# Kernel tuning notes

Measured on AMD Instinct MI355X. Metric: run time of the kernel, lower is better.

## Reference

```python
import jax, jax.numpy as jnp
import numpy as np

B, T, D, H = 2, 2048, 1024, 16
HD = D // H
FF = 4 * D
EPS = 1e-5


def rmsnorm(x, w):
    var = jnp.mean(jnp.square(x), axis=-1, keepdims=True)
    return x * jax.lax.rsqrt(var + EPS) * w


def setup_inputs() -> dict:
    key = jax.random.key(0)
    ks = jax.random.split(key, 17)
    sc = 0.02
    d = {}
    d["x"] = jax.random.normal(ks[0], (B, T, D), jnp.float32)
    d["x_token"] = jax.random.normal(ks[1], (B, T, D), jnp.float32)
    d["pos_emb"] = jax.random.normal(ks[2], (T, D), jnp.float32)
    d["lc_weight"] = jax.random.normal(ks[3], (1,), jnp.float32)
    d["Wq"] = jax.random.normal(ks[4], (D, D), jnp.float32) * sc  # per-head query weights stacked
    d["Wk"] = jax.random.normal(ks[5], (D, D), jnp.float32) * sc
    d["Wv"] = jax.random.normal(ks[6], (D, D), jnp.float32) * sc
    d["proj_w"] = jax.random.normal(ks[7], (D, D), jnp.float32) * sc
    d["proj_b"] = jnp.zeros((D,), jnp.float32)
    d["w1_w"] = jax.random.normal(ks[8], (FF, D), jnp.float32) * sc
    d["w1_b"] = jnp.zeros((FF,), jnp.float32)
    d["w2_w"] = jax.random.normal(ks[9], (D, FF), jnp.float32) * sc
    d["w2_b"] = jnp.zeros((D,), jnp.float32)
    d["w3_w"] = jax.random.normal(ks[10], (FF, D), jnp.float32) * sc
    d["w3_b"] = jnp.zeros((FF,), jnp.float32)
    d["norm1_w"] = jnp.ones((D,), jnp.float32)
    d["norm2_w"] = jnp.ones((D,), jnp.float32)
    return d


def reference(x, x_token, pos_emb, lc_weight, Wq, Wk, Wv, proj_w, proj_b,
              w1_w, w1_b, w2_w, w2_b, w3_w, w3_b, norm1_w, norm2_w):
    lc = jax.nn.sigmoid(lc_weight)  # scalar gate
    x_att = lc * x + (1.0 - lc) * x_token
    xn = rmsnorm(x_att, norm1_w)

    # q, v from normed gated input; k from raw positional embedding (faithful to source)
    q = (xn @ Wq.T).reshape(B, T, H, HD)
    k = (pos_emb @ Wk.T).reshape(T, H, HD)
    v = (xn @ Wv.T).reshape(B, T, H, HD)

    # NOTE: scale uses full model dim E (=D), not head_size, as in the source
    scores = jnp.einsum('bqhd,khd->bhqk', q, k) * (D ** -0.5)
    causal = jnp.tril(jnp.ones((T, T), bool))
    scores = jnp.where(causal, scores, -jnp.inf)
    p = jax.nn.softmax(scores, axis=-1)
    attn = jnp.einsum('bhqk,bkhd->bqhd', p, v).reshape(B, T, D)

    x = x + attn @ proj_w.T + proj_b

    xn2 = rmsnorm(x, norm2_w)
    h = jax.nn.silu(xn2 @ w1_w.T + w1_b) * (xn2 @ w3_w.T + w3_b)
    return x + h @ w2_w.T + w2_b
```

## Files before the change

kernel.cpp:

```cpp
#include <hip/hip_runtime.h>
#include <hip/hip_bf16.h>


typedef __hip_bfloat16 bf16;
typedef __attribute__((ext_vector_type(8))) short bf16x8;
typedef __attribute__((ext_vector_type(4))) float floatx4;

constexpr int cB = 2, cT = 2048, cD = 1024, cH = 16, cFF = 4096;
constexpr float cEPS = 1e-5f;
constexpr unsigned BF16_ONES = 0x3F803F80u;

__device__ __forceinline__ float b2f(bf16 x) { return __bfloat162float(x); }
__device__ __forceinline__ bf16  f2b(float x) { return __float2bfloat16(x); }
__device__ __forceinline__ unsigned short f2bu(float x) {
  bf16 t = __float2bfloat16(x);
  union { bf16 b; unsigned short u; } cv;
  cv.b = t;
  return cv.u;
}
__device__ __forceinline__ float loadR(const bf16* p)  { return b2f(*p); }
__device__ __forceinline__ float loadR(const float* p) { return *p; }

__device__ __forceinline__ void gload16(const bf16* g, unsigned short* l) {
  __builtin_amdgcn_global_load_lds(
      (const __attribute__((address_space(1))) void*)g,
      (__attribute__((address_space(3))) void*)l, 16, 0, 0);
}

__device__ __forceinline__ int xcd_remap1(int lin, int n) {
  return (lin & 7) * (n >> 3) + (lin >> 3);
}

struct ConvArgs {
  const void* src[17];
  bf16* dst[17];
  int n[17];
  int sb[17];
};

__global__ __launch_bounds__(256) void convert_all_k(ConvArgs a) {
  const int bid = blockIdx.x;
  int seg = 0;
#pragma unroll
  for (int i = 1; i < 17; i++) seg = (bid >= a.sb[i]) ? i : seg;
  const int n = a.n[seg];
  const int i0 = (bid - a.sb[seg]) * 2048 + threadIdx.x * 8;
  if (i0 >= n) return;
  const bool isb = (((const unsigned*)a.src[15])[0] == BF16_ONES);
  const void* src = a.src[seg];
  bf16* dst = a.dst[seg];
  if (i0 + 8 <= n) {
    if (isb) {
      *(int4*)(dst + i0) = *(const int4*)((const bf16*)src + i0);
    } else {
      float4 f0 = *(const float4*)((const float*)src + i0);
      float4 f1 = *(const float4*)((const float*)src + i0 + 4);
      int4 ro;
      bf16* po = (bf16*)&ro;
      po[0] = f2b(f0.x); po[1] = f2b(f0.y); po[2] = f2b(f0.z); po[3] = f2b(f0.w);
      po[4] = f2b(f1.x); po[5] = f2b(f1.y); po[6] = f2b(f1.z); po[7] = f2b(f1.w);
      *(int4*)(dst + i0) = ro;
    }
  } else {
    for (int j = i0; j < n; j++)
      dst[j] = isb ? ((const bf16*)src)[j] : f2b(((const float*)src)[j]);
  }
}

template <int OUTK, typename ResT>
__device__ __forceinline__ void gemm_core64(
    const bf16* __restrict__ A, const bf16* __restrict__ W,
    const bf16* __restrict__ bias, const ResT* __restrict__ R,
    void* __restrict__ Cv,
    int N, int Kst, int kb, int klen, int m0, int n0,
    unsigned short* As, unsigned short* Bs)
{
  const int tid  = threadIdx.x;
  const int wave = tid >> 6;
  const int lane = tid & 63;
  const int l15  = lane & 15;
  const int quad = lane >> 4;
  const int wm   = (wave >> 1) * 64;
  const int wn   = (wave & 1) * 32;

  const int lr  = lane >> 2;
  const int lc8 = (lane & 3) * 8;
  const bf16* Ag0 = A + (size_t)(m0 + wave * 32 + lr) * Kst + kb + lc8;
  const bf16* Ag1 = Ag0 + (size_t)16 * Kst;
  const bf16* Bg0 = W + (size_t)(n0 + wave * 16 + lr) * Kst + kb + lc8;
  unsigned short* lA0 = &As[(wave * 32) * 32];
  unsigned short* lA1 = &As[(wave * 32 + 16) * 32];
  unsigned short* lB0 = &Bs[(wave * 16) * 32];

  floatx4 acc[4][2];
#pragma unroll
  for (int i = 0; i < 4; i++)
#pragma unroll
    for (int j = 0; j < 2; j++) acc[i][j] = (floatx4){0.f, 0.f, 0.f, 0.f};

  for (int k0 = 0; k0 < klen; k0 += 64) {
    gload16(Ag0 + k0, lA0);
    gload16(Ag1 + k0, lA1);
    gload16(Ag0 + k0 + 32, lA0 + 128 * 32);
    gload16(Ag1 + k0 + 32, lA1 + 128 * 32);
    gload16(Bg0 + k0, lB0);
    gload16(Bg0 + k0 + 32, lB0 + 64 * 32);
    __syncthreads();

    bf16x8 a[4][2], b[2][2];
#pragma unroll
    for (int t = 0; t < 4; t++)
#pragma unroll
      for (int kh = 0; kh < 2; kh++)
        a[t][kh] = *(const bf16x8*)&As[kh * 128 * 32 + (wm + t * 16 + l15) * 32 + quad * 8];
#pragma unroll
    for (int u = 0; u < 2; u++)
#pragma unroll
      for (int kh = 0; kh < 2; kh++)
        b[u][kh] = *(const bf16x8*)&Bs[kh * 64 * 32 + (wn + u * 16 + l15) * 32 + quad * 8];
#pragma unroll
    for (int tm = 0; tm < 4; tm++)
#pragma unroll
      for (int tn = 0; tn < 2; tn++)
#pragma unroll
        for (int kh = 0; kh < 2; kh++)
          acc[tm][tn] = __builtin_amdgcn_mfma_f32_16x16x32_bf16(a[tm][kh], b[tn][kh], acc[tm][tn], 0, 0, 0);
    __syncthreads();
  }

#pragma unroll
  for (int tm = 0; tm < 4; tm++) {
#pragma unroll
    for (int tn = 0; tn < 2; tn++) {
      const int row = m0 + wm + tm * 16 + quad * 4;
      const int col = n0 + wn + tn * 16 + l15;
      float bv = (OUTK != 3 && bias) ? b2f(bias[col]) : 0.f;
#pragma unroll
      for (int i = 0; i < 4; i++) {
        float val = acc[tm][tn][i] + bv;
        const size_t cidx = (size_t)(row + i) * N + col;
        if (OUTK == 3) {
          atomicAdd((float*)Cv + cidx, val);
        } else if (OUTK == 4) {
          ((bf16*)Cv)[(size_t)col * (size_t)(cB * cT) + (row + i)] = f2b(val);
        } else {
          if (R) val += loadR(&R[cidx]);
          if (OUTK == 0) ((bf16*)Cv)[cidx] = f2b(val);
          else           ((float*)Cv)[cidx] = val;
        }
      }
    }
  }
}

template <int OUTK, typename ResT>
__global__ __launch_bounds__(256) void gemm_f(
    const bf16* __restrict__ A, const bf16* __restrict__ W,
    const bf16* __restrict__ bias, const ResT* __restrict__ R,
    void* __restrict__ Cv, int N, int Kst, int kchunk, int gx, int gxy)
{
  __shared__ __align__(16) unsigned short As[2 * 128 * 32];
  __shared__ __align__(16) unsigned short Bs[2 * 64 * 32];
  const int lin = xcd_remap1(blockIdx.x, gridDim.x);
  const int kz  = lin / gxy;
  const int rem = lin % gxy;
  gemm_core64<OUTK, ResT>(A, W, bias, R, Cv, N, Kst, kz * kchunk, kchunk,
                          (rem / gx) * 128, (rem % gx) * 64, As, Bs);
}

__global__ __launch_bounds__(256) void gemm_qkv(
    const bf16* __restrict__ xn, const bf16* __restrict__ pos,
    const bf16* __restrict__ Wq, const bf16* __restrict__ Wv,
    const bf16* __restrict__ Wk,
    bf16* __restrict__ q, bf16* __restrict__ vT, bf16* __restrict__ kb)
{
  __shared__ __align__(16) unsigned short As[2 * 128 * 32];
  __shared__ __align__(16) unsigned short Bs[2 * 64 * 32];
  const int lin = xcd_remap1(blockIdx.x, gridDim.x);
  int z, local;
  if (lin < 512)       { z = 0; local = lin; }
  else if (lin < 1024) { z = 1; local = lin - 512; }
  else                 { z = 2; local = lin - 1024; }
  const int gx = 16;
  const int by = local / gx, bx = local % gx;
  if (z == 1) {
    gemm_core64<4, bf16>(xn, Wv, nullptr, (const bf16*)nullptr, vT,
                         cD, cD, 0, cD, by * 128, bx * 64, As, Bs);
  } else {
    const bf16* A = (z == 2) ? pos : xn;
    const bf16* W = (z == 0) ? Wq : Wk;
    bf16* C = (z == 0) ? q : kb;
    gemm_core64<0, bf16>(A, W, nullptr, (const bf16*)nullptr, C,
                         cD, cD, 0, cD, by * 128, bx * 64, As, Bs);
  }
}

template <int MODE>
__global__ __launch_bounds__(512, 2) void gemm8p(
    const bf16* __restrict__ A, const bf16* __restrict__ W,
    const bf16* __restrict__ bias, bf16* H)
{
  __shared__ __align__(16) unsigned short As[2 * 2 * 256 * 32];
  __shared__ __align__(16) unsigned short Bs[2 * 2 * 256 * 32];
  constexpr int K = cD;
  constexpr int NT = K / 64;
  const int lin = xcd_remap1(blockIdx.x, gridDim.x);
  const int by = lin >> 4, bx = lin & 15;
  const int m0 = by * 256, n0 = bx * 256;

  const int tid  = threadIdx.x;
  const int wave = tid >> 6;
  const int lane = tid & 63;
  const int l15  = lane & 15;
  const int quad = lane >> 4;
  const int wm   = wave >> 2;
  const int wq   = wave & 3;
  const int swz  = (quad ^ (l15 & 3) ^ ((l15 >> 2) & 3)) * 8;

  const int srow = wave * 32 + (lane >> 2);
  const int sblk = (lane & 3) ^ ((lane >> 2) & 3) ^ ((lane >> 4) & 3);
  const bf16* Ags = A + (size_t)(m0 + srow) * K + sblk * 8;
  const bf16* Wgs = W + (size_t)(n0 + srow) * K + sblk * 8;
  unsigned short* const lA = &As[0] + (wave * 32) * 32;
  unsigned short* const lB = &Bs[0] + (wave * 32) * 32;

  floatx4 acc[8][4];
#pragma unroll
  for (int i = 0; i < 8; i++)
#pragma unroll
    for (int j = 0; j < 4; j++) acc[i][j] = (floatx4){0.f, 0.f, 0.f, 0.f};

#define STAGE_A8(buf, kel, kh)                                              \
  { const bf16* s_ = Ags + (kel) + (kh) * 32;                               \
    unsigned short* d_ = lA + (buf) * (2 * 256 * 32) + (kh) * (256 * 32);   \
    gload16(s_, d_);                                                        \
    gload16(s_ + (size_t)16 * K, d_ + 16 * 32); }
#define STAGE_B8(buf, kel, kh)                                              \
  { const bf16* s_ = Wgs + (kel) + (kh) * 32;                               \
    unsigned short* d_ = lB + (buf) * (2 * 256 * 32) + (kh) * (256 * 32);   \
    gload16(s_, d_);                                                        \
    gload16(s_ + (size_t)16 * K, d_ + 16 * 32); }

#define WAITBAR4()                                                          \
  asm volatile("s_waitcnt vmcnt(4)" ::: "memory");                          \
  __builtin_amdgcn_sched_barrier(0);                                        \
  __builtin_amdgcn_s_barrier();                                             \
  __builtin_amdgcn_sched_barrier(0);

  STAGE_A8(0, 0, 0); STAGE_B8(0, 0, 0); STAGE_A8(0, 0, 1); STAGE_B8(0, 0, 1);
  asm volatile("s_waitcnt vmcnt(0)" ::: "memory");
  __builtin_amdgcn_sched_barrier(0);
  __builtin_amdgcn_s_barrier();
  __builtin_amdgcn_sched_barrier(0);

  int buf = 0;
#pragma unroll 1
  for (int t = 0; t < NT; ++t) {
    const int nkel = (t + 1) * 64;
    const bool pf = (t + 1 < NT);
    const unsigned short* ab = &As[0] + buf * (2 * 256 * 32);
    const unsigned short* bb = &Bs[0] + buf * (2 * 256 * 32);
    bf16x8 bfr[4], af[4];

    WAITBAR4();
#pragma unroll
    for (int nf = 0; nf < 4; nf++)
      bfr[nf] = *(const bf16x8*)&bb[(wq * 64 + nf * 16 + l15) * 32 + swz];
#pragma unroll
    for (int j = 0; j < 4; j++)
      af[j] = *(const bf16x8*)&ab[(wm * 128 + j * 16 + l15) * 32 + swz];
    __builtin_amdgcn_sched_barrier(0);
    if (pf) STAGE_A8(buf ^ 1, nkel, 0);
    __builtin_amdgcn_s_setprio(1);
#pragma unroll
    for (int j = 0; j < 4; j++)
#pragma unroll
      for (int nf = 0; nf < 4; nf++)
        acc[j][nf] = __builtin_amdgcn_mfma_f32_16x16x32_bf16(af[j], bfr[nf], acc[j][nf], 0, 0, 0);
    __builtin_amdgcn_s_setprio(0);

#pragma unroll
    for (int j = 0; j < 4; j++)
      af[j] = *(const bf16x8*)&ab[(wm * 128 + 64 + j * 16 + l15) * 32 + swz];
    __builtin_amdgcn_sched_barrier(0);
    if (pf) STAGE_B8(buf ^ 1, nkel, 0);
    __builtin_amdgcn_s_setprio(1);
#pragma unroll
    for (int j = 0; j < 4; j++)
#pragma unroll
      for (int nf = 0; nf < 4; nf++)
        acc[4 + j][nf] = __builtin_amdgcn_mfma_f32_16x16x32_bf16(af[j], bfr[nf], acc[4 + j][nf], 0, 0, 0);
    __builtin_amdgcn_s_setprio(0);

    WAITBAR4();
#pragma unroll
    for (int nf = 0; nf < 4; nf++)
      bfr[nf] = *(const bf16x8*)&bb[256 * 32 + (wq * 64 + nf * 16 + l15) * 32 + swz];
#pragma unroll
    for (int j = 0; j < 4; j++)
      af[j] = *(const bf16x8*)&ab[256 * 32 + (wm * 128 + j * 16 + l15) * 32 + swz];
    __builtin_amdgcn_sched_barrier(0);
    if (pf) STAGE_A8(buf ^ 1, nkel, 1);
    __builtin_amdgcn_s_setprio(1);
#pragma unroll
    for (int j = 0; j < 4; j++)
#pragma unroll
      for (int nf = 0; nf < 4; nf++)
        acc[j][nf] = __builtin_amdgcn_mfma_f32_16x16x32_bf16(af[j], bfr[nf], acc[j][nf], 0, 0, 0);
    __builtin_amdgcn_s_setprio(0);

#pragma unroll
    for (int j = 0; j < 4; j++)
      af[j] = *(const bf16x8*)&ab[256 * 32 + (wm * 128 + 64 + j * 16 + l15) * 32 + swz];
    __builtin_amdgcn_sched_barrier(0);
    if (pf) STAGE_B8(buf ^ 1, nkel, 1);
    __builtin_amdgcn_s_setprio(1);
#pragma unroll
    for (int j = 0; j < 4; j++)
#pragma unroll
      for (int nf = 0; nf < 4; nf++)
        acc[4 + j][nf] = __builtin_amdgcn_mfma_f32_16x16x32_bf16(af[j], bfr[nf], acc[4 + j][nf], 0, 0, 0);
    __builtin_amdgcn_s_setprio(0);

    buf ^= 1;
  }
#undef STAGE_A8
#undef STAGE_B8
#undef WAITBAR4

#pragma unroll
  for (int mf = 0; mf < 8; mf++) {
#pragma unroll
    for (int nf = 0; nf < 4; nf++) {
      const int row = m0 + wm * 128 + mf * 16 + quad * 4;
      const int col = n0 + wq * 64 + nf * 16 + l15;
      const float bv = b2f(bias[col]);
#pragma unroll
      for (int i = 0; i < 4; i++) {
        const size_t idx = (size_t)(row + i) * cFF + col;
        float v = acc[mf][nf][i] + bv;
        if (MODE == 0) {
          v = v * (1.f / (1.f + __expf(-v)));
          H[idx] = f2b(v);
        } else {
          H[idx] = f2b(v * b2f(H[idx]));
        }
      }
    }
  }
}

template <bool GATE, typename InT>
__global__ __launch_bounds__(256) void rmsnorm_k(
    const InT* __restrict__ X, const bf16* __restrict__ XT,
    const bf16* __restrict__ LC, const bf16* __restrict__ Wn,
    bf16* __restrict__ O, float* __restrict__ Z)
{
  const int row = blockIdx.x;
  const int tid = threadIdx.x;
  const size_t base = (size_t)row * cD;
  const int c = tid * 4;

  if (Z) *(float4*)(Z + base + c) = (float4){0.f, 0.f, 0.f, 0.f};

  float lc = 1.f, lc1 = 0.f;
  if (GATE) {
    float g = b2f(LC[0]);
    lc = 1.f / (1.f + __expf(-g));
    lc1 = 1.f - lc;
  }

  float xv[4];
  if (sizeof(InT) == 2) {
    ushort4 u = *(const ushort4*)((const unsigned short*)X + base + c);
    const bf16* pu = (const bf16*)&u;
#pragma unroll
    for (int i = 0; i < 4; i++) xv[i] = b2f(pu[i]);
  } else {
    float4 f = *(const float4*)((const float*)X + base + c);
    xv[0] = f.x; xv[1] = f.y; xv[2] = f.z; xv[3] = f.w;
  }
  if (GATE) {
    ushort4 u = *(const ushort4*)((const unsigned short*)XT + base + c);
    const bf16* pu = (const bf16*)&u;
#pragma unroll
    for (int i = 0; i < 4; i++) xv[i] = lc * xv[i] + lc1 * b2f(pu[i]);
  }

  float ss = xv[0] * xv[0] + xv[1] * xv[1] + xv[2] * xv[2] + xv[3] * xv[3];
#pragma unroll
  for (int off = 32; off; off >>= 1) ss += __shfl_xor(ss, off, 64);

  __shared__ float red[4];
  if ((tid & 63) == 0) red[tid >> 6] = ss;
  __syncthreads();
  float tot = red[0] + red[1] + red[2] + red[3];
  float rs = rsqrtf(tot * (1.f / cD) + cEPS);

  ushort4 o;
  bf16* po = (bf16*)&o;
#pragma unroll
  for (int i = 0; i < 4; i++) po[i] = f2b(xv[i] * rs * b2f(Wn[c + i]));
  *(ushort4*)((unsigned short*)O + base + c) = o;
}

__global__ __launch_bounds__(256) void combine_k(
    const float* __restrict__ P, const float* __restrict__ X2,
    const bf16* __restrict__ bias, void* __restrict__ out,
    const unsigned* __restrict__ dbits)
{
  const bool obf = (*dbits == BF16_ONES);
  const size_t idx = ((size_t)blockIdx.x * 256 + threadIdx.x) * 4;
  float4 p = *(const float4*)(P + idx);
  float4 x = *(const float4*)(X2 + idx);
  const int col = (int)(idx & (cD - 1));
  ushort4 bu = *(const ushort4*)((const unsigned short*)bias + col);
  const bf16* bb = (const bf16*)&bu;
  float v0 = p.x + x.x + b2f(bb[0]);
  float v1 = p.y + x.y + b2f(bb[1]);
  float v2 = p.z + x.z + b2f(bb[2]);
  float v3 = p.w + x.w + b2f(bb[3]);
  if (obf) {
    ushort4 o;
    bf16* po = (bf16*)&o;
    po[0] = f2b(v0); po[1] = f2b(v1); po[2] = f2b(v2); po[3] = f2b(v3);
    *(ushort4*)((unsigned short*)out + idx) = o;
  } else {
    *(float4*)((float*)out + idx) = (float4){v0, v1, v2, v3};
  }
}

__global__ __launch_bounds__(256) void fattn_k(
    const bf16* __restrict__ Q, const bf16* __restrict__ K,
    const bf16* __restrict__ Vt, bf16* __restrict__ O)
{
  constexpr int LQ = 72;
  constexpr int BT = cB * cT;
  __shared__ __align__(16) unsigned short Qs[64 * LQ];
  __shared__ __align__(16) unsigned short Ks[2 * 64 * 64];
  __shared__ __align__(16) unsigned short Vs[2 * 64 * 64];

  const int tid  = threadIdx.x;
  const int wave = tid >> 6;
  const int lane = tid & 63;
  const int l15  = lane & 15;
  const int quad = lane >> 4;
  const int blk  = blockIdx.x;
  const int qt   = 31 - (blk & 31);
  const int h    = (blk >> 5) & 15;
  const int b    = blk >> 9;
  const int q0   = qt * 64;

  const bf16* Qb = Q + ((size_t)b * cT) * cD + h * 64;
  const bf16* Kb = K + h * 64;
  const bf16* Vb = Vt + (size_t)(h * 64) * BT + (size_t)b * cT;

  const int sr = lane >> 3;
  const int sc = ((lane & 7) ^ sr) * 8;
  unsigned short* const kd = &Ks[0] + wave * 512;
  unsigned short* const vd = &Vs[0] + wave * 512;

  auto STAGE = [&](int bf, int k0) {
    const bf16* ks = Kb + (size_t)(k0 + wave * 8 + sr) * cD + sc;
    gload16(ks,           kd + bf * 4096);
    gload16(ks + 32 * cD, kd + bf * 4096 + 2048);
    const bf16* vs = Vb + (size_t)(wave * 8 + sr) * BT + k0 + sc;
    gload16(vs,                   vd + bf * 4096);
    gload16(vs + (size_t)32 * BT, vd + bf * 4096 + 2048);
  };

  const int ktiles = qt + 1;
  STAGE(0, 0);

  {
    const int qr = tid >> 2, qc = (tid & 3) * 16;
    const bf16* gq = Qb + (size_t)(q0 + qr) * cD + qc;
    *(int4*)&Qs[qr * LQ + qc]     = *(const int4*)(gq);
    *(int4*)&Qs[qr * LQ + qc + 8] = *(const int4*)(gq + 8);
  }
  __syncthreads();

  const int qw = wave * 16;
  bf16x8 qa[2];
#pragma unroll
  for (int dc = 0; dc < 2; dc++)
    qa[dc] = *(const bf16x8*)&Qs[(qw + l15) * LQ + dc * 32 + quad * 8];

  float l_p[4] = {0.f, 0.f, 0.f, 0.f};
  floatx4 oacc[4];
#pragma unroll
  for (int dt = 0; dt < 4; dt++) oacc[dt] = (floatx4){0.f, 0.f, 0.f, 0.f};

  unsigned short* Pw = &Qs[qw * LQ];
  const int swk = l15 & 7;
  const int rb0 = (quad ^ swk) * 8;
  const int rb1 = ((quad + 4) ^ swk) * 8;

  int bf = 0;
  for (int it = 0; it < ktiles; ++it) {
    const int k0 = it * 64;
    if (it + 1 < ktiles) STAGE(bf ^ 1, k0 + 64);

    const unsigned short* kb_ = &Ks[bf * 4096];
    const unsigned short* vb_ = &Vs[bf * 4096];

    floatx4 s[4];
#pragma unroll
    for (int st = 0; st < 4; st++) {
      bf16x8 kb0 = *(const bf16x8*)&kb_[(st * 16 + l15) * 64 + rb0];
      bf16x8 kb1 = *(const bf16x8*)&kb_[(st * 16 + l15) * 64 + rb1];
      s[st] = (floatx4){0.f, 0.f, 0.f, 0.f};
      s[st] = __builtin_amdgcn_mfma_f32_16x16x32_bf16(qa[0], kb0, s[st], 0, 0, 0);
      s[st] = __builtin_amdgcn_mfma_f32_16x16x32_bf16(qa[1], kb1, s[st], 0, 0, 0);
    }
    float p[4][4];
#pragma unroll
    for (int i = 0; i < 4; i++) {
      const int qrow = q0 + qw + quad * 4 + i;
#pragma unroll
      for (int st = 0; st < 4; st++) {
        const int kp = k0 + st * 16 + l15;
        float pv = (kp > qrow) ? 0.f : __expf(s[st][i] * 0.03125f);
        p[st][i] = pv;
        l_p[i] += pv;
      }
    }
#pragma unroll
    for (int st = 0; st < 4; st++)
#pragma unroll
      for (int i = 0; i < 4; i++)
        Pw[(quad * 4 + i) * LQ + st * 16 + l15] = f2bu(p[st][i]);
    bf16x8 pa[2];
#pragma unroll
    for (int pc = 0; pc < 2; pc++)
      pa[pc] = *(const bf16x8*)&Pw[l15 * LQ + pc * 32 + quad * 8];
#pragma unroll
    for (int dt = 0; dt < 4; dt++) {
      bf16x8 vb0 = *(const bf16x8*)&vb_[(dt * 16 + l15) * 64 + rb0];
      bf16x8 vb1 = *(const bf16x8*)&vb_[(dt * 16 + l15) * 64 + rb1];
      oacc[dt] = __builtin_amdgcn_mfma_f32_16x16x32_bf16(pa[0], vb0, oacc[dt], 0, 0, 0);
      oacc[dt] = __builtin_amdgcn_mfma_f32_16x16x32_bf16(pa[1], vb1, oacc[dt], 0, 0, 0);
    }

    __syncthreads();
    bf ^= 1;
  }

  float rl[4];
#pragma unroll
  for (int i = 0; i < 4; i++) {
    float li = l_p[i];
#pragma unroll
    for (int off = 1; off < 16; off <<= 1) li += __shfl_xor(li, off, 64);
    rl[i] = 1.f / li;
  }
  const size_t obase = ((size_t)b * cT + q0 + qw) * cD + h * 64;
#pragma unroll
  for (int dt = 0; dt < 4; dt++)
#pragma unroll
    for (int i = 0; i < 4; i++)
      O[obase + (size_t)(quad * 4 + i) * cD + dt * 16 + l15] = f2b(oacc[dt][i] * rl[i]);
}

extern "C" void kernel_launch(void* const* d_in, const int* in_sizes, int n_in,
                              void* d_out, int out_size, void* d_ws, size_t ws_size,
                              hipStream_t stream) {
  char* ws = (char*)d_ws;
  const size_t MB = 1u << 20;
  const int BT = cB * cT;

  bf16* cxt  = (bf16*)(ws + 0);
  bf16* cpos = (bf16*)(ws + 8 * MB);
  bf16* q    = (bf16*)(ws + 12 * MB);
  bf16* kbuf = (bf16*)(ws + 20 * MB);
  bf16* vT   = (bf16*)(ws + 24 * MB);
  bf16* h    = (bf16*)(ws + 0);
  size_t off = 32 * MB;
  auto alloc = [&](size_t bytes) -> char* {
    char* p = ws + off;
    off = (off + bytes + 255) & ~(size_t)255;
    return p;
  };
  bf16*  cx  = (bf16*)alloc((size_t)BT * cD * 2);
  bf16*  xn  = (bf16*)alloc((size_t)BT * cD * 2);
  float* x2  = (float*)alloc((size_t)BT * cD * 4);
  bf16*  xn2 = (bf16*)alloc((size_t)BT * cD * 2);
  float* part = (float*)(ws + 32 * MB);
  bf16* cin[17];
  cin[0] = cx; cin[1] = cxt; cin[2] = cpos;
  for (int i = 3; i < 17; i++) cin[i] = (bf16*)alloc((size_t)in_sizes[i] * 2);

  const unsigned* dbits = (const unsigned*)d_in[15];
  dim3 blk(256);

  ConvArgs ca;
  int nblk = 0;
  for (int i = 0; i < 17; i++) {
    ca.src[i] = d_in[i];
    ca.dst[i] = cin[i];
    ca.n[i] = in_sizes[i];
    ca.sb[i] = nblk;
    nblk += (in_sizes[i] + 2047) / 2048;
  }
  convert_all_k<<<nblk, blk, 0, stream>>>(ca);

  const bf16 *clc = cin[3], *cWq = cin[4], *cWk = cin[5], *cWv = cin[6];
  const bf16 *cprojw = cin[7], *cprojb = cin[8];
  const bf16 *cw1w = cin[9], *cw1b = cin[10], *cw2w = cin[11], *cw2b = cin[12];
  const bf16 *cw3w = cin[13], *cw3b = cin[14], *cn1 = cin[15], *cn2 = cin[16];

  rmsnorm_k<true, bf16><<<BT, blk, 0, stream>>>(cx, cxt, clc, cn1, xn, nullptr);
  gemm_qkv<<<1280, blk, 0, stream>>>(xn, cpos, cWq, cWv, cWk, q, vT, kbuf);
  bf16* attn = xn;
  fattn_k<<<cB * cH * (cT / 64), blk, 0, stream>>>(q, kbuf, vT, attn);
  gemm_f<1, bf16><<<512, blk, 0, stream>>>(
      attn, cprojw, cprojb, cx, x2, cD, cD, cD, 16, 512);
  rmsnorm_k<false, float><<<BT, blk, 0, stream>>>(
      x2, (const bf16*)nullptr, (const bf16*)nullptr, cn2, xn2, part);
  gemm8p<0><<<256, 512, 0, stream>>>(xn2, cw1w, cw1b, h);
  gemm8p<1><<<256, 512, 0, stream>>>(xn2, cw3w, cw3b, h);
  gemm_f<3, float><<<1024, blk, 0, stream>>>(
      h, cw2w, nullptr, (const float*)nullptr, part, cD, cFF, 2048, 16, 512);
  combine_k<<<BT, blk, 0, stream>>>(part, x2, cw2b, d_out, dbits);
  (void)n_in; (void)out_size; (void)ws_size;
}
```

Measured before the change: 464.1 us.

## Fuse W1 and W3 FFN GEMMs into one SwiGLU kernel

Merges the two separate FFN up-projection GEMM launches into a single kernel. Each block computes a 256x128 tile of both the W1 and W3 products, sharing the A tile, and applies silu(g)*u in the epilogue. This removes the second pass over xn2, the write-then-read of the intermediate h for the gating multiply, and one launch. In exchange it uses 512 blocks with narrower N tiles and swaps the block index mapping (by/bx). It also adds an XCD remap of block indices to the attention kernel.

```diff
diff --git a/kernel.cpp b/kernel.cpp
--- a/kernel.cpp
+++ b/kernel.cpp
@@ -195,18 +195,21 @@
   }
 }
 
-template <int MODE>
-__global__ __launch_bounds__(512, 2) void gemm8p(
-    const bf16* __restrict__ A, const bf16* __restrict__ W,
-    const bf16* __restrict__ bias, bf16* H)
+__global__ __launch_bounds__(512, 2) void gemm8pf(
+    const bf16* __restrict__ A,
+    const bf16* __restrict__ W1, const bf16* __restrict__ b1,
+    const bf16* __restrict__ W3, const bf16* __restrict__ b3,
+    bf16* __restrict__ H)
 {
   __shared__ __align__(16) unsigned short As[2 * 2 * 256 * 32];
-  __shared__ __align__(16) unsigned short Bs[2 * 2 * 256 * 32];
+  __shared__ __align__(16) unsigned short B1s[2 * 2 * 128 * 32];
+  __shared__ __align__(16) unsigned short B3s[2 * 2 * 128 * 32];
   constexpr int K = cD;
   constexpr int NT = K / 64;
   const int lin = xcd_remap1(blockIdx.x, gridDim.x);
-  const int by = lin >> 4, bx = lin & 15;
-  const int m0 = by * 256, n0 = bx * 256;
+  const int by = lin & 15;
+  const int bx = lin >> 4;
+  const int m0 = by * 256, n0 = bx * 128;
 
   const int tid  = threadIdx.x;
   const int wave = tid >> 6;
@@ -217,18 +220,24 @@
   const int wq   = wave & 3;
   const int swz  = (quad ^ (l15 & 3) ^ ((l15 >> 2) & 3)) * 8;
 
-  const int srow = wave * 32 + (lane >> 2);
-  const int sblk = (lane & 3) ^ ((lane >> 2) & 3) ^ ((lane >> 4) & 3);
-  const bf16* Ags = A + (size_t)(m0 + srow) * K + sblk * 8;
-  const bf16* Wgs = W + (size_t)(n0 + srow) * K + sblk * 8;
-  unsigned short* const lA = &As[0] + (wave * 32) * 32;
-  unsigned short* const lB = &Bs[0] + (wave * 32) * 32;
-
-  floatx4 acc[8][4];
+  const int srowA = wave * 32 + (lane >> 2);
+  const int sblk  = (lane & 3) ^ ((lane >> 2) & 3) ^ ((lane >> 4) & 3);
+  const bf16* Ags = A + (size_t)(m0 + srowA) * K + sblk * 8;
+  const int srowB = wave * 16 + (lane >> 2);
+  const bf16* W1gs = W1 + (size_t)(n0 + srowB) * K + sblk * 8;
+  const bf16* W3gs = W3 + (size_t)(n0 + srowB) * K + sblk * 8;
+  unsigned short* const lA  = &As[0]  + (wave * 32) * 32;
+  unsigned short* const lB1 = &B1s[0] + (wave * 16) * 32;
+  unsigned short* const lB3 = &B3s[0] + (wave * 16) * 32;
+
+  floatx4 acc1[8][2], acc3[8][2];
 #pragma unroll
   for (int i = 0; i < 8; i++)
 #pragma unroll
-    for (int j = 0; j < 4; j++) acc[i][j] = (floatx4){0.f, 0.f, 0.f, 0.f};
+    for (int j = 0; j < 2; j++) {
+      acc1[i][j] = (floatx4){0.f, 0.f, 0.f, 0.f};
+      acc3[i][j] = (floatx4){0.f, 0.f, 0.f, 0.f};
+    }
 
 #define STAGE_A8(buf, kel, kh)                                              \
   { const bf16* s_ = Ags + (kel) + (kh) * 32;                               \
@@ -236,10 +245,10 @@
     gload16(s_, d_);                                                        \
     gload16(s_ + (size_t)16 * K, d_ + 16 * 32); }
 #define STAGE_B8(buf, kel, kh)                                              \
-  { const bf16* s_ = Wgs + (kel) + (kh) * 32;                               \
-    unsigned short* d_ = lB + (buf) * (2 * 256 * 32) + (kh) * (256 * 32);   \
-    gload16(s_, d_);                                                        \
-    gload16(s_ + (size_t)16 * K, d_ + 16 * 32); }
+  { gload16(W1gs + (kel) + (kh) * 32,                                       \
+            lB1 + (buf) * (2 * 128 * 32) + (kh) * (128 * 32));              \
+    gload16(W3gs + (kel) + (kh) * 32,                                       \
+            lB3 + (buf) * (2 * 128 * 32) + (kh) * (128 * 32)); }
 
 #define WAITBAR4()                                                          \
   asm volatile("s_waitcnt vmcnt(4)" ::: "memory");                          \
@@ -258,14 +267,17 @@
   for (int t = 0; t < NT; ++t) {
     const int nkel = (t + 1) * 64;
     const bool pf = (t + 1 < NT);
-    const unsigned short* ab = &As[0] + buf * (2 * 256 * 32);
-    const unsigned short* bb = &Bs[0] + buf * (2 * 256 * 32);
-    bf16x8 bfr[4], af[4];
+    const unsigned short* ab  = &As[0]  + buf * (2 * 256 * 32);
+    const unsigned short* bb1 = &B1s[0] + buf * (2 * 128 * 32);
+    const unsigned short* bb3 = &B3s[0] + buf * (2 * 128 * 32);
+    bf16x8 bf1[2], bf3[2], af[4];
 
     WAITBAR4();
 #pragma unroll
-    for (int nf = 0; nf < 4; nf++)
-      bfr[nf] = *(const bf16x8*)&bb[(wq * 64 + nf * 16 + l15) * 32 + swz];
+    for (int nf = 0; nf < 2; nf++) {
+      bf1[nf] = *(const bf16x8*)&bb1[(wq * 32 + nf * 16 + l15) * 32 + swz];
+      bf3[nf] = *(const bf16x8*)&bb3[(wq * 32 + nf * 16 + l15) * 32 + swz];
+    }
 #pragma unroll
     for (int j = 0; j < 4; j++)
       af[j] = *(const bf16x8*)&ab[(wm * 128 + j * 16 + l15) * 32 + swz];
@@ -275,8 +287,10 @@
 #pragma unroll
     for (int j = 0; j < 4; j++)
 #pragma unroll
-      for (int nf = 0; nf < 4; nf++)
-        acc[j][nf] = __builtin_amdgcn_mfma_f32_16x16x32_bf16(af[j], bfr[nf], acc[j][nf], 0, 0, 0);
+      for (int nf = 0; nf < 2; nf++) {
+        acc1[j][nf] = __builtin_amdgcn_mfma_f32_16x16x32_bf16(af[j], bf1[nf], acc1[j][nf], 0, 0, 0);
+        acc3[j][nf] = __builtin_amdgcn_mfma_f32_16x16x32_bf16(af[j], bf3[nf], acc3[j][nf], 0, 0, 0);
+      }
     __builtin_amdgcn_s_setprio(0);
 
 #pragma unroll
@@ -288,14 +302,18 @@
 #pragma unroll
     for (int j = 0; j < 4; j++)
 #pragma unroll
-      for (int nf = 0; nf < 4; nf++)
-        acc[4 + j][nf] = __builtin_amdgcn_mfma_f32_16x16x32_bf16(af[j], bfr[nf], acc[4 + j][nf], 0, 0, 0);
+      for (int nf = 0; nf < 2; nf++) {
+        acc1[4 + j][nf] = __builtin_amdgcn_mfma_f32_16x16x32_bf16(af[j], bf1[nf], acc1[4 + j][nf], 0, 0, 0);
+        acc3[4 + j][nf] = __builtin_amdgcn_mfma_f32_16x16x32_bf16(af[j], bf3[nf], acc3[4 + j][nf], 0, 0, 0);
+      }
     __builtin_amdgcn_s_setprio(0);
 
     WAITBAR4();
 #pragma unroll
-    for (int nf = 0; nf < 4; nf++)
-      bfr[nf] = *(const bf16x8*)&bb[256 * 32 + (wq * 64 + nf * 16 + l15) * 32 + swz];
+    for (int nf = 0; nf < 2; nf++) {
+      bf1[nf] = *(const bf16x8*)&bb1[128 * 32 + (wq * 32 + nf * 16 + l15) * 32 + swz];
+      bf3[nf] = *(const bf16x8*)&bb3[128 * 32 + (wq * 32 + nf * 16 + l15) * 32 + swz];
+    }
 #pragma unroll
     for (int j = 0; j < 4; j++)
       af[j] = *(const bf16x8*)&ab[256 * 32 + (wm * 128 + j * 16 + l15) * 32 + swz];
@@ -305,8 +323,10 @@
 #pragma unroll
     for (int j = 0; j < 4; j++)
 #pragma unroll
-      for (int nf = 0; nf < 4; nf++)
-        acc[j][nf] = __builtin_amdgcn_mfma_f32_16x16x32_bf16(af[j], bfr[nf], acc[j][nf], 0, 0, 0);
+      for (int nf = 0; nf < 2; nf++) {
+        acc1[j][nf] = __builtin_amdgcn_mfma_f32_16x16x32_bf16(af[j], bf1[nf], acc1[j][nf], 0, 0, 0);
+        acc3[j][nf] = __builtin_amdgcn_mfma_f32_16x16x32_bf16(af[j], bf3[nf], acc3[j][nf], 0, 0, 0);
+      }
     __builtin_amdgcn_s_setprio(0);
 
 #pragma unroll
@@ -318,8 +338,10 @@
 #pragma unroll
     for (int j = 0; j < 4; j++)
 #pragma unroll
-      for (int nf = 0; nf < 4; nf++)
-        acc[4 + j][nf] = __builtin_amdgcn_mfma_f32_16x16x32_bf16(af[j], bfr[nf], acc[4 + j][nf], 0, 0, 0);
+      for (int nf = 0; nf < 2; nf++) {
+        acc1[4 + j][nf] = __builtin_amdgcn_mfma_f32_16x16x32_bf16(af[j], bf1[nf], acc1[4 + j][nf], 0, 0, 0);
+        acc3[4 + j][nf] = __builtin_amdgcn_mfma_f32_16x16x32_bf16(af[j], bf3[nf], acc3[4 + j][nf], 0, 0, 0);
+      }
     __builtin_amdgcn_s_setprio(0);
 
     buf ^= 1;
@@ -331,20 +353,17 @@
 #pragma unroll
   for (int mf = 0; mf < 8; mf++) {
 #pragma unroll
-    for (int nf = 0; nf < 4; nf++) {
+    for (int nf = 0; nf < 2; nf++) {
       const int row = m0 + wm * 128 + mf * 16 + quad * 4;
-      const int col = n0 + wq * 64 + nf * 16 + l15;
-      const float bv = b2f(bias[col]);
+      const int col = n0 + wq * 32 + nf * 16 + l15;
+      const float bv1 = b2f(b1[col]);
+      const float bv3 = b2f(b3[col]);
 #pragma unroll
       for (int i = 0; i < 4; i++) {
-        const size_t idx = (size_t)(row + i) * cFF + col;
-        float v = acc[mf][nf][i] + bv;
-        if (MODE == 0) {
-          v = v * (1.f / (1.f + __expf(-v)));
-          H[idx] = f2b(v);
-        } else {
-          H[idx] = f2b(v * b2f(H[idx]));
-        }
+        float g = acc1[mf][nf][i] + bv1;
+        float u = acc3[mf][nf][i] + bv3;
+        float v = g * (1.f / (1.f + __expf(-g))) * u;
+        H[(size_t)(row + i) * cFF + col] = f2b(v);
       }
     }
   }
@@ -445,7 +464,7 @@
   const int lane = tid & 63;
   const int l15  = lane & 15;
   const int quad = lane >> 4;
-  const int blk  = blockIdx.x;
+  const int blk  = xcd_remap1(blockIdx.x, gridDim.x);
   const int qt   = 31 - (blk & 31);
   const int h    = (blk >> 5) & 15;
   const int b    = blk >> 9;
@@ -617,8 +636,7 @@
       attn, cprojw, cprojb, cx, x2, cD, cD, cD, 16, 512);
   rmsnorm_k<false, float><<<BT, blk, 0, stream>>>(
       x2, (const bf16*)nullptr, (const bf16*)nullptr, cn2, xn2, part);
-  gemm8p<0><<<256, 512, 0, stream>>>(xn2, cw1w, cw1b, h);
-  gemm8p<1><<<256, 512, 0, stream>>>(xn2, cw3w, cw3b, h);
+  gemm8pf<<<512, 512, 0, stream>>>(xn2, cw1w, cw1b, cw3w, cw3b, h);
   gemm_f<3, float><<<1024, blk, 0, stream>>>(
       h, cw2w, nullptr, (const float*)nullptr, part, cD, cFF, 2048, 16, 512);
   combine_k<<<BT, blk, 0, stream>>>(part, x2, cw2b, d_out, dbits);
```

Measured after the change: 428.4 us. 7.7% less time.
